# Kernel tuning notes

Hardware: AMD Instinct MI355X
Metric: run time of the kernel (lower is better)

## Reference

```python
import jax, jax.numpy as jnp
import numpy as np

V, E, H, C = 100000, 300, 512, 3
SP, SH, B = 64, 32, 128


def lstm_scan(x, Wih, Whh, b):
    # x: [T, B, E]; PyTorch gate order i, f, g, o
    T, Bb, _ = x.shape
    Hh = Whh.shape[1]
    h0 = jnp.zeros((Bb, Hh), x.dtype)

    def step(carry, xt):
        h, c = carry
        g = xt @ Wih.T + h @ Whh.T + b
        i, f, gg, o = jnp.split(g, 4, axis=-1)
        c = jax.nn.sigmoid(f) * c + jax.nn.sigmoid(i) * jnp.tanh(gg)
        h = jax.nn.sigmoid(o) * jnp.tanh(c)
        return (h, c), h

    _, hs = jax.lax.scan(step, (h0, h0), x)
    return hs  # [T, B, H]


def setup_inputs() -> dict:
    key = jax.random.key(0)
    ks = jax.random.split(key, 20)
    inv_sqrt_h = 1.0 / np.sqrt(H).astype(np.float32)

    def u(k, shape, scale):
        return (jax.random.uniform(k, shape, jnp.float32) * 2.0 - 1.0) * scale

    embed_table = jax.random.normal(ks[4], (V, E), jnp.float32) * 0.1
    embed_table = embed_table.at[0].set(0.0)  # padding_idx=0
    return {
        "premise": jax.random.randint(ks[0], (SP, B), 1, V),
        "premise_len": jax.random.randint(ks[1], (B,), 1, SP + 1),
        "hypothesis": jax.random.randint(ks[2], (SH, B), 1, V),
        "hypothesis_len": jax.random.randint(ks[3], (B,), 1, SH + 1),
        "embed_table": embed_table,
        "p_Wih": u(ks[5], (4 * H, E), inv_sqrt_h),
        "p_Whh": u(ks[6], (4 * H, H), inv_sqrt_h),
        "p_b": u(ks[7], (4 * H,), inv_sqrt_h),
        "h_Wih": u(ks[8], (4 * H, E), inv_sqrt_h),
        "h_Whh": u(ks[9], (4 * H, H), inv_sqrt_h),
        "h_b": u(ks[10], (4 * H,), inv_sqrt_h),
        "m_Wih": u(ks[11], (4 * H, 2 * H), inv_sqrt_h),
        "m_Whh": u(ks[12], (4 * H, H), inv_sqrt_h),
        "m_b": u(ks[13], (4 * H,), inv_sqrt_h),
        "w_e": jax.random.uniform(ks[14], (H,), jnp.float32),
        "Ws": u(ks[15], (H, H), np.sqrt(6.0 / (2 * H)).astype(np.float32)),
        "Wt": u(ks[16], (H, H), np.sqrt(6.0 / (2 * H)).astype(np.float32)),
        "Wm": u(ks[17], (H, H), np.sqrt(6.0 / (2 * H)).astype(np.float32)),
        "fc_W": u(ks[18], (C, H), np.sqrt(6.0 / (H + C)).astype(np.float32)),
        "fc_b": jnp.zeros((C,), jnp.float32),
    }


def reference(premise, premise_len, hypothesis, hypothesis_len, embed_table,
              p_Wih, p_Whh, p_b, h_Wih, h_Whh, h_b, m_Wih, m_Whh, m_b,
              w_e, Ws, Wt, Wm, fc_W, fc_b):
    Sp, Bb = premise.shape
    Sh = hypothesis.shape[0]
    Hh = Ws.shape[0]

    # Encoder LSTMs; emulate pack/pad: outputs past length are zeros
    h_s = lstm_scan(embed_table[premise], p_Wih, p_Whh, p_b)  # [Sp,B,H]
    h_s = h_s * (jnp.arange(Sp)[:, None] < premise_len[None, :]).astype(h_s.dtype)[:, :, None]
    h_t = lstm_scan(embed_table[hypothesis], h_Wih, h_Whh, h_b)  # [Sh,B,H]
    h_t = h_t * (jnp.arange(Sh)[:, None] < hypothesis_len[None, :]).astype(h_t.dtype)[:, :, None]

    Ws_hs = jnp.einsum('sbe,he->sbh', h_s, Ws)  # precompute premise projection

    def step(carry, inputs):
        h_m, c_m, h_last = carry
        h_t_k, k = inputs
        q = h_t_k @ Wt.T + h_m @ Wm.T                              # [B,H]
        e = jnp.einsum('sbh,h->sb', jnp.tanh(Ws_hs + q[None]), w_e)  # [Sp,B]
        alpha = jax.nn.softmax(e, axis=0)                           # softmax over premise (no mask, as in original)
        a_k = jnp.einsum('sb,sbh->bh', alpha, h_s)
        m_k = jnp.concatenate([a_k, h_t_k], axis=1)                 # [B,2H]
        g = m_k @ m_Wih.T + h_m @ m_Whh.T + m_b
        i, f, gg, o = jnp.split(g, 4, axis=-1)
        c_new = jax.nn.sigmoid(f) * c_m + jax.nn.sigmoid(i) * jnp.tanh(gg)
        h_new = jax.nn.sigmoid(o) * jnp.tanh(c_new)
        h_last = jnp.where((k + 1 == hypothesis_len)[:, None], h_new, h_last)
        return (h_new, c_new, h_last), None

    z = jnp.zeros((Bb, Hh), h_s.dtype)
    (_, _, h_last), _ = jax.lax.scan(step, (z, z, z), (h_t, jnp.arange(Sh)))
    return h_last @ fc_W.T + fc_b  # [B, C]
```

## Files before the change

### kernel.cpp

```cpp
#include <hip/hip_runtime.h>


#define NWG 256
#define TPB 512

typedef float f8v __attribute__((ext_vector_type(8)));

#define O_XPP      0ull
#define O_HTMW     0ull
#define O_HTWT     8388608ull
#define O_WSHS     10485760ull
#define O_XPH      16777216ull
#define O_HST      25165824ull
#define O_HS2      29360128ull
#define O_HTT      33554432ull
#define O_WIHTP    35651584ull
#define O_WIHTH    36265984ull
#define O_WHHPP    36880384ull
#define O_WHHPH    37928960ull
#define O_DW       38977536ull
#define O_WST      41074688ull
#define O_WTT      41336832ull
#define O_MWIHRT   41598976ull
#define O_BPP      42647552ull
#define O_BPH      42649600ull
#define O_BPM      42651648ull
#define O_HT2      42653696ull
#define O_HMT2     42784768ull
#define O_QBUF     42915840ull
#define O_AK2      42981376ull
#define O_HLAST    43046912ull
#define WS_FLOATS  43112448ull

__device__ unsigned g_FE[NWG * 16];
__device__ unsigned g_FA[NWG * 16];
__device__ unsigned g_FB[NWG * 16];
__device__ unsigned g_FD[NWG * 16];

struct Params {
  const int* premise; const int* plen; const int* hyp; const int* hlen;
  const float* embed;
  const float* pWih; const float* pWhh; const float* pb;
  const float* hWih; const float* hWhh; const float* hb;
  const float* mWih; const float* mWhh; const float* mb;
  const float* we; const float* Ws; const float* Wt; const float* Wm;
  const float* fcW; const float* fcb;
  float* out; float* ws;
};

__device__ __forceinline__ float2 sysld2(const float* p){
  unsigned long long u = __hip_atomic_load((const unsigned long long*)p,
      __ATOMIC_RELAXED, __HIP_MEMORY_SCOPE_SYSTEM);
  union { unsigned long long u; float2 f; } c; c.u = u; return c.f;
}
__device__ __forceinline__ void sysst(float* p, float v){
  union { float f; unsigned u; } c; c.f = v;
  __hip_atomic_store((unsigned*)p, c.u, __ATOMIC_RELAXED, __HIP_MEMORY_SCOPE_SYSTEM);
}
__device__ __forceinline__ void fbump(unsigned* a, unsigned v){
  __hip_atomic_store(a, v, __ATOMIC_RELAXED, __HIP_MEMORY_SCOPE_SYSTEM);
}
__device__ __forceinline__ unsigned fread_(const unsigned* a){
  return __hip_atomic_load(a, __ATOMIC_RELAXED, __HIP_MEMORY_SCOPE_SYSTEM);
}
__device__ __forceinline__ void waitflag(const unsigned* a, unsigned tgt){
  while ((int)(fread_(a) - tgt) < 0) __builtin_amdgcn_s_sleep(2);
}

__device__ __forceinline__ float sigf(float x){ return 1.0f/(1.0f + __expf(-x)); }
__device__ __forceinline__ float tanhf_(float x){ return 2.0f/(1.0f + __expf(-2.0f*x)) - 1.0f; }

__device__ __forceinline__ float wsum(float v){
  #pragma unroll
  for (int o = 32; o > 0; o >>= 1) v += __shfl_xor(v, o, 64);
  return v;
}
__device__ __forceinline__ float wmaxr(float v){
  #pragma unroll
  for (int o = 32; o > 0; o >>= 1) v = fmaxf(v, __shfl_xor(v, o, 64));
  return v;
}

__global__ __launch_bounds__(TPB) void k_s0(Params p){
  const int tid0 = blockIdx.x * TPB + threadIdx.x;
  const int stride = gridDim.x * TPB;
  float* const ws = p.ws;
  float* const WihTp  = ws + O_WIHTP;
  float* const WihTh  = ws + O_WIHTH;
  float* const WhhPP  = ws + O_WHHPP;
  float* const WhhPH  = ws + O_WHHPH;
  float* const DW     = ws + O_DW;
  float* const WsT    = ws + O_WST;
  float* const WtT    = ws + O_WTT;
  float* const mWihRT = ws + O_MWIHRT;
  float* const bpP    = ws + O_BPP;
  float* const bpH    = ws + O_BPH;
  float* const bpM    = ws + O_BPM;

  for (int idx = tid0; idx < 300*2048; idx += stride){
    int e = idx >> 11, jp = idx & 2047;
    int oc = (jp & 3) * 512 + (jp >> 2);
    WihTp[idx] = p.pWih[(size_t)oc*300 + e];
    WihTh[idx] = p.hWih[(size_t)oc*300 + e];
  }
  for (int idx = tid0; idx < 1024*512*2; idx += stride){
    int g = idx & 1, k = (idx >> 1) & 511, pp = idx >> 10;
    int hc = pp >> 1, gp = pp & 1, oc = (gp*2+g)*512 + hc;
    WhhPP[idx] = p.pWhh[(size_t)oc*512 + k];
    WhhPH[idx] = p.hWhh[(size_t)oc*512 + k];
  }
  for (int idx = tid0; idx < 1024*1024*2; idx += stride){
    int g = idx & 1, k = (idx >> 1) & 1023, pp = idx >> 11;
    int hc = pp >> 1, gp = pp & 1, oc = (gp*2+g)*512 + hc;
    DW[idx] = (k < 512) ? p.mWih[(size_t)oc*1024 + k]
                        : p.mWhh[(size_t)oc*512 + (k - 512)];
  }
  for (int idx = tid0; idx < 512*512; idx += stride){
    int k = idx >> 9, h = idx & 511;
    WsT[idx] = p.Ws[(size_t)h*512 + k];
    WtT[idx] = p.Wt[(size_t)h*512 + k];
  }
  for (int idx = tid0; idx < 512*2048; idx += stride){
    int k = idx >> 11, jp = idx & 2047;
    int oc = (jp & 3) * 512 + (jp >> 2);
    mWihRT[idx] = p.mWih[(size_t)oc*1024 + 512 + k];
  }
  for (int idx = tid0; idx < 2048; idx += stride){
    int oc = (idx & 3) * 512 + (idx >> 2);
    bpP[idx] = p.pb[oc]; bpH[idx] = p.hb[oc]; bpM[idx] = p.mb[oc];
  }
}

__global__ __launch_bounds__(TPB) void k_s1(Params p){
  const int tid = threadIdx.x, lane = tid & 63, wave = tid >> 6;
  const int gwave = blockIdx.x * 8 + wave;
  const int wstride = gridDim.x * 8;
  float* const ws = p.ws;
  float* const XPp   = ws + O_XPP;
  float* const XPh   = ws + O_XPH;
  const float* WihTp = ws + O_WIHTP;
  const float* WihTh = ws + O_WIHTH;
  const float* bpP   = ws + O_BPP;
  const float* bpH   = ws + O_BPH;

  for (int task = gwave; task < 6144; task += wstride){
    const bool prem = task < 4096;
    int rb, cb;
    if (prem){ cb = task >> 10; rb = task & 1023; }
    else { int t2 = task - 4096; cb = t2 >> 9; rb = t2 & 511; }
    const int r0 = rb * 8;
    const int* toks = prem ? p.premise : p.hyp;
    const float* wT = prem ? WihTp : WihTh;
    const float* bias = prem ? bpP : bpH;
    float* outp = prem ? XPp : XPh;
    const int j0 = cb * 512 + lane * 8;
    const float* xr[8];
    #pragma unroll
    for (int r = 0; r < 8; ++r) xr[r] = p.embed + (size_t)toks[r0 + r] * 300;
    f8v bias8 = *(const f8v*)(bias + j0);
    float acc[8][8];
    #pragma unroll
    for (int r = 0; r < 8; ++r){
      #pragma unroll
      for (int i = 0; i < 8; ++i) acc[r][i] = 0.f;
    }
    for (int e = 0; e < 300; ++e){
      f8v w8 = *(const f8v*)(wT + (size_t)e * 2048 + j0);
      #pragma unroll
      for (int r = 0; r < 8; ++r){
        float xv = xr[r][e];
        #pragma unroll
        for (int i = 0; i < 8; ++i) acc[r][i] += xv * w8[i];
      }
    }
    #pragma unroll
    for (int r = 0; r < 8; ++r){
      f8v o8;
      #pragma unroll
      for (int i = 0; i < 8; ++i) o8[i] = acc[r][i] + bias8[i];
      *(f8v*)(outp + (size_t)(r0 + r) * 2048 + j0) = o8;
    }
  }
}

__device__ void lstm_enc(int wg, int tid, int cg, int bg, int T,
    const float* __restrict__ XP, const float* __restrict__ WPair,
    const int* __restrict__ lens, float* hbuf,
    float* __restrict__ houtT, float* __restrict__ hout2, float* lds,
    unsigned B)
{
  const int b8 = tid & 7, hc32 = (tid >> 3) & 31, gp = tid >> 8;
  const int b = bg*8 + b8, hc = cg*32 + hc32;
  const float* wrow = WPair + (size_t)(hc*2 + gp) * 1024;
  const int mylen = lens[b];
  const int sb = tid >> 6, sk = (tid & 63) * 8;
  float* stage = lds;
  float* xch   = lds + 8*516;
  float c_reg = 0.f;

  for (int t = 0; t < T; ++t){
    const float* hin  = hbuf + (size_t)(t & 1) * 65536;
    float*       hout = hbuf + (size_t)((t + 1) & 1) * 65536;
    if (t > 0){
      if (tid < 16) waitflag(&g_FE[(unsigned)(bg*16 + tid)*16], B + t);
      __syncthreads();
      const float* src = hin + (size_t)(bg*8 + sb)*512 + sk;
      float2 v0 = sysld2(src), v1 = sysld2(src+2), v2 = sysld2(src+4), v3 = sysld2(src+6);
      float* dst = stage + sb*516 + sk;
      float4 w0 = {v0.x, v0.y, v1.x, v1.y};
      float4 w1 = {v2.x, v2.y, v3.x, v3.y};
      *(float4*)dst = w0; *(float4*)(dst+4) = w1;
    }
    __syncthreads();
    float a0 = 0.f, a1 = 0.f;
    if (t > 0){
      const float* hr = stage + b8*516;
      #pragma unroll 2
      for (int k = 0; k < 512; k += 4){
        float4 h4 = *(const float4*)(hr + k);
        float4 wA = *(const float4*)(wrow + k*2);
        float4 wB = *(const float4*)(wrow + k*2 + 4);
        a0 += h4.x*wA.x + h4.y*wA.z + h4.z*wB.x + h4.w*wB.z;
        a1 += h4.x*wA.y + h4.y*wA.w + h4.z*wB.y + h4.w*wB.w;
      }
    }
    float2 xg = *(const float2*)(XP + ((size_t)t*128 + b)*2048 + hc*4 + gp*2);
    a0 += xg.x; a1 += xg.y;
    if (gp == 1){ xch[(b8*32+hc32)*2+0] = a0; xch[(b8*32+hc32)*2+1] = a1; }
    __syncthreads();
    if (gp == 0){
      float gg = xch[(b8*32+hc32)*2+0], go = xch[(b8*32+hc32)*2+1];
      float iv = sigf(a0), fv = sigf(a1), gv = tanhf_(gg), ov = sigf(go);
      c_reg = fv * c_reg + iv * gv;
      float hv = ov * tanhf_(c_reg);
      sysst(hout + (size_t)b*512 + hc, hv);
      float hm = (t < mylen) ? hv : 0.f;
      houtT[((size_t)t*512 + hc)*128 + b] = hm;
      if (hout2) hout2[((size_t)t*128 + b)*512 + hc] = hm;
    }
    __syncthreads();
    if (tid == 0) fbump(&g_FE[wg*16], B + t + 1);
  }
}

__global__ __launch_bounds__(TPB, 2) void k_encp(Params p){
  const int wg = blockIdx.x, tid = threadIdx.x;
  const int cg = wg & 15, bg = wg >> 4;
  __shared__ float lds[4640];
  __shared__ unsigned shB;
  if (tid == 0) shB = fread_(&g_FE[wg*16]);
  __syncthreads();
  lstm_enc(wg, tid, cg, bg, 64, p.ws + O_XPP, p.ws + O_WHHPP, p.plen,
           p.ws + O_HT2, p.ws + O_HST, p.ws + O_HS2, lds, shB);
}
__global__ __launch_bounds__(TPB, 2) void k_ench(Params p){
  const int wg = blockIdx.x, tid = threadIdx.x;
  const int cg = wg & 15, bg = wg >> 4;
  __shared__ float lds[4640];
  __shared__ unsigned shB;
  if (tid == 0) shB = fread_(&g_FE[wg*16]);
  __syncthreads();
  lstm_enc(wg, tid, cg, bg, 32, p.ws + O_XPH, p.ws + O_WHHPH, p.hlen,
           p.ws + O_HT2, p.ws + O_HTT, nullptr, lds, shB);
}

__global__ __launch_bounds__(TPB) void k_s4(Params p){
  const int tid = threadIdx.x, lane = tid & 63, wave = tid >> 6;
  const int gwave = blockIdx.x * 8 + wave;
  const int wstride = gridDim.x * 8;
  float* const ws = p.ws;
  const float* h_sT   = ws + O_HST;
  const float* h_tT   = ws + O_HTT;
  const float* WsT    = ws + O_WST;
  const float* WtT    = ws + O_WTT;
  const float* mWihRT = ws + O_MWIHRT;
  const float* bpM    = ws + O_BPM;
  float* const Ws_hs  = ws + O_WSHS;
  float* const htWt   = ws + O_HTWT;
  float* const htmW   = ws + O_HTMW;

  for (int task = gwave; task < 3584; task += wstride){
    const float* src; const float* wT; const float* bias; float* outp;
    int rb, cb, cols;
    if (task < 1024){ rb = task;        cb = 0;            src = h_sT; wT = WsT;    bias = nullptr; outp = Ws_hs; cols = 512; }
    else if (task < 1536){ rb = task-1024; cb = 0;         src = h_tT; wT = WtT;    bias = nullptr; outp = htWt;  cols = 512; }
    else { int t2 = task - 1536; cb = t2 >> 9; rb = t2 & 511; src = h_tT; wT = mWihRT; bias = bpM;  outp = htmW;  cols = 2048; }
    const int r0 = rb * 8;
    const int j0 = cb * 512 + lane * 8;
    const float* xr[8];
    #pragma unroll
    for (int r = 0; r < 8; ++r){
      int row = r0 + r;
      xr[r] = src + (size_t)(row >> 7) * 65536 + (row & 127);
    }
    f8v bias8 = {0,0,0,0,0,0,0,0};
    if (bias) bias8 = *(const f8v*)(bias + j0);
    float acc[8][8];
    #pragma unroll
    for (int r = 0; r < 8; ++r){
      #pragma unroll
      for (int i = 0; i < 8; ++i) acc[r][i] = 0.f;
    }
    for (int k = 0; k < 512; ++k){
      f8v w8 = *(const f8v*)(wT + (size_t)k * cols + j0);
      #pragma unroll
      for (int r = 0; r < 8; ++r){
        float xv = xr[r][(size_t)k * 128];
        #pragma unroll
        for (int i = 0; i < 8; ++i) acc[r][i] += xv * w8[i];
      }
    }
    #pragma unroll
    for (int r = 0; r < 8; ++r){
      f8v o8;
      #pragma unroll
      for (int i = 0; i < 8; ++i) o8[i] = acc[r][i] + bias8[i];
      *(f8v*)(outp + (size_t)(r0 + r) * (size_t)cols + j0) = o8;
    }
  }
}

__global__ __launch_bounds__(TPB, 2) void k_match(Params p){
  const int wg = blockIdx.x, tid = threadIdx.x;
  const int lane = tid & 63, wave = tid >> 6;
  const int cg = wg & 15, bg = wg >> 4;
  __shared__ float lds[8736];
  __shared__ unsigned shB;
  if (tid == 0) shB = fread_(&g_FD[wg*16]);
  __syncthreads();
  const unsigned B = shB;

  float* const ws = p.ws;
  const float* htmW  = ws + O_HTMW;
  const float* htWt  = ws + O_HTWT;
  const float* Ws_hs = ws + O_WSHS;
  const float* h_s2  = ws + O_HS2;
  const float* DW    = ws + O_DW;
  float* const hmT2  = ws + O_HMT2;
  float* const qbuf  = ws + O_QBUF;
  float* const ak2   = ws + O_AK2;
  float* const hlast = ws + O_HLAST;

  const int b8 = tid & 7, hc32 = (tid >> 3) & 31, gp = tid >> 8;
  const int mb_ = bg*8 + b8, mhc = cg*32 + hc32;
  const float* dwrow = DW + (size_t)(mhc*2 + gp) * 2048;
  const int hyplen_b = p.hlen[mb_];
  const int sb = tid >> 6, sk = (tid & 63) * 8;
  float* stage  = lds;
  float* xchA   = lds + 8*516;
  float* stage2 = lds;
  float* xch2   = lds + 8*1028;
  float cm_reg = 0.f, hl_reg = 0.f;

  for (int k = 0; k < 32; ++k){
    const float* hmin  = hmT2 + (size_t)(k & 1) * 65536;
    float*       hmout = hmT2 + (size_t)((k + 1) & 1) * 65536;

    if (tid < 16) waitflag(&g_FD[(unsigned)(bg*16 + tid)*16], B + k);
    else if (tid < 24) waitflag(&g_FB[(unsigned)(bg*8 + tid - 16)*16], B + k);
    __syncthreads();
    if (k > 0){
      const float* src = hmin + (size_t)(bg*8 + sb)*512 + sk;
      float2 v0 = sysld2(src), v1 = sysld2(src+2), v2 = sysld2(src+4), v3 = sysld2(src+6);
      float* dst = stage + sb*516 + sk;
      float4 w0 = {v0.x, v0.y, v1.x, v1.y};
      float4 w1 = {v2.x, v2.y, v3.x, v3.y};
      *(float4*)dst = w0; *(float4*)(dst+4) = w1;
    }
    __syncthreads();
    {
      const int c32 = (tid >> 3) & 31, half = tid >> 8;
      const int c = cg*32 + c32;
      float a = 0.f;
      if (k > 0){
        const float* hr = stage + b8*516 + half*256;
        const float* wr = p.Wm + (size_t)c*512 + half*256;
        #pragma unroll 2
        for (int kk = 0; kk < 256; kk += 4){
          float4 h4 = *(const float4*)(hr + kk);
          float4 w4 = *(const float4*)(wr + kk);
          a += h4.x*w4.x + h4.y*w4.y + h4.z*w4.z + h4.w*w4.w;
        }
      }
      if (half == 1) xchA[c32*8 + b8] = a;
      __syncthreads();
      if (half == 0){
        float v = a + xchA[c32*8 + b8] + htWt[((size_t)k*128 + mb_)*512 + c];
        sysst(qbuf + (size_t)mb_*512 + c, v);
      }
    }
    __syncthreads();
    if (tid == 0) fbump(&g_FA[wg*16], B + k + 1);

    if (wg < 128){
      const int bb = wg;
      if (tid < 16) waitflag(&g_FA[(unsigned)((bb >> 3)*16 + tid)*16], B + k + 1);
      else if (tid < 32) waitflag(&g_FD[(unsigned)((bb >> 3)*16 + tid - 16)*16], B + k);
      __syncthreads();
      const float* qb = qbuf + (size_t)bb*512 + lane*8;
      float2 qa = sysld2(qb), qbv = sysld2(qb+2), qc = sysld2(qb+4), qd = sysld2(qb+6);
      float4 q0 = {qa.x, qa.y, qbv.x, qbv.y};
      float4 q1 = {qc.x, qc.y, qd.x, qd.y};
      float4 e0 = *(const float4*)(p.we + lane*8);
      float4 e1 = *(const float4*)(p.we + lane*8 + 4);
      #pragma unroll
      for (int si = 0; si < 8; ++si){
        int s = wave*8 + si;
        const float* wsr = Ws_hs + ((size_t)s*128 + bb)*512 + lane*8;
        float4 s0 = *(const float4*)wsr;
        float4 s1 = *(const float4*)(wsr + 4);
        float v = tanhf_(s0.x + q0.x)*e0.x + tanhf_(s0.y + q0.y)*e0.y
                + tanhf_(s0.z + q0.z)*e0.z + tanhf_(s0.w + q0.w)*e0.w
                + tanhf_(s1.x + q1.x)*e1.x + tanhf_(s1.y + q1.y)*e1.y
                + tanhf_(s1.z + q1.z)*e1.z + tanhf_(s1.w + q1.w)*e1.w;
        v = wsum(v);
        if (lane == 0) lds[s] = v;
      }
      __syncthreads();
      if (wave == 0){
        float v = lds[lane];
        float m = wmaxr(v);
        float ex = __expf(v - m);
        float sm = wsum(ex);
        lds[64 + lane] = ex / sm;
      }
      __syncthreads();
      {
        float acc = 0.f;
        const float* hsb = h_s2 + (size_t)bb*512 + tid;
        #pragma unroll 4
        for (int s = 0; s < 64; s += 4){
          float4 al = *(const float4*)(lds + 64 + s);
          acc += al.x * hsb[(size_t)(s+0)*65536]
               + al.y * hsb[(size_t)(s+1)*65536]
               + al.z * hsb[(size_t)(s+2)*65536]
               + al.w * hsb[(size_t)(s+3)*65536];
        }
        sysst(ak2 + (size_t)bb*512 + tid, acc);
      }
      __syncthreads();
      if (tid == 0) fbump(&g_FB[wg*16], B + k + 1);
    }

    if (tid < 8) waitflag(&g_FB[(unsigned)(bg*8 + tid)*16], B + k + 1);
    __syncthreads();
    {
      const int sb2 = tid >> 6, c0 = (tid & 63) * 16;
      float* dst = stage2 + sb2*1028 + c0;
      if (c0 < 512){
        const float* src = ak2 + (size_t)(bg*8 + sb2)*512 + c0;
        #pragma unroll
        for (int i = 0; i < 16; i += 4){
          float2 va = sysld2(src + i), vb = sysld2(src + i + 2);
          float4 w = {va.x, va.y, vb.x, vb.y};
          *(float4*)(dst + i) = w;
        }
      } else if (k > 0){
        const float* src = hmin + (size_t)(bg*8 + sb2)*512 + (c0 - 512);
        #pragma unroll
        for (int i = 0; i < 16; i += 4){
          float2 va = sysld2(src + i), vb = sysld2(src + i + 2);
          float4 w = {va.x, va.y, vb.x, vb.y};
          *(float4*)(dst + i) = w;
        }
      } else {
        float4 z = {0.f, 0.f, 0.f, 0.f};
        #pragma unroll
        for (int i = 0; i < 16; i += 4) *(float4*)(dst + i) = z;
      }
    }
    __syncthreads();
    {
      float a0 = 0.f, a1 = 0.f;
      const float* hr = stage2 + b8*1028;
      #pragma unroll 2
      for (int kk = 0; kk < 1024; kk += 4){
        float4 h4 = *(const float4*)(hr + kk);
        float4 wA = *(const float4*)(dwrow + kk*2);
        float4 wB = *(const float4*)(dwrow + kk*2 + 4);
        a0 += h4.x*wA.x + h4.y*wA.z + h4.z*wB.x + h4.w*wB.z;
        a1 += h4.x*wA.y + h4.y*wA.w + h4.z*wB.y + h4.w*wB.w;
      }
      float2 xg = *(const float2*)(htmW + ((size_t)k*128 + mb_)*2048 + mhc*4 + gp*2);
      a0 += xg.x; a1 += xg.y;
      if (gp == 1){ xch2[(b8*32+hc32)*2+0] = a0; xch2[(b8*32+hc32)*2+1] = a1; }
      __syncthreads();
      if (gp == 0){
        float gg = xch2[(b8*32+hc32)*2+0], go = xch2[(b8*32+hc32)*2+1];
        float iv = sigf(a0), fv = sigf(a1), gv = tanhf_(gg), ov = sigf(go);
        cm_reg = fv * cm_reg + iv * gv;
        float hv = ov * tanhf_(cm_reg);
        sysst(hmout + (size_t)mb_*512 + mhc, hv);
        if (k + 1 == hyplen_b) hl_reg = hv;
      }
    }
    __syncthreads();
    if (tid == 0) fbump(&g_FD[wg*16], B + k + 1);
  }

  if (gp == 0) sysst(hlast + (size_t)mb_*512 + mhc, hl_reg);
  __syncthreads();
  if (tid == 0){
    fbump(&g_FD[wg*16], B + 40);
    fbump(&g_FA[wg*16], B + 40);
    fbump(&g_FB[wg*16], B + 40);
  }

  if (wg == 0){
    if (tid < NWG) waitflag(&g_FD[(unsigned)tid*16], B + 40);
    __syncthreads();
    for (int o = wave; o < 384; o += 8){
      int bb = o / 3, cls = o - bb*3;
      const float* hr = hlast + (size_t)bb*512 + lane*8;
      const float* wr = p.fcW + (size_t)cls*512 + lane*8;
      float2 ha = sysld2(hr), hb = sysld2(hr+2), hc2 = sysld2(hr+4), hd = sysld2(hr+6);
      float4 w0 = *(const float4*)wr, w1 = *(const float4*)(wr + 4);
      float v = ha.x*w0.x + ha.y*w0.y + hb.x*w0.z + hb.y*w0.w
              + hc2.x*w1.x + hc2.y*w1.y + hd.x*w1.z + hd.y*w1.w;
      v = wsum(v);
      if (lane == 0) p.out[o] = v + p.fcb[cls];
    }
  }
}

extern "C" void kernel_launch(void* const* d_in, const int* in_sizes, int n_in,
                              void* d_out, int out_size, void* d_ws, size_t ws_size,
                              hipStream_t stream) {
  if (ws_size < WS_FLOATS * sizeof(float)) return;
  Params prm;
  prm.premise = (const int*)d_in[0];
  prm.plen    = (const int*)d_in[1];
  prm.hyp     = (const int*)d_in[2];
  prm.hlen    = (const int*)d_in[3];
  prm.embed   = (const float*)d_in[4];
  prm.pWih    = (const float*)d_in[5];
  prm.pWhh    = (const float*)d_in[6];
  prm.pb      = (const float*)d_in[7];
  prm.hWih    = (const float*)d_in[8];
  prm.hWhh    = (const float*)d_in[9];
  prm.hb      = (const float*)d_in[10];
  prm.mWih    = (const float*)d_in[11];
  prm.mWhh    = (const float*)d_in[12];
  prm.mb      = (const float*)d_in[13];
  prm.we      = (const float*)d_in[14];
  prm.Ws      = (const float*)d_in[15];
  prm.Wt      = (const float*)d_in[16];
  prm.Wm      = (const float*)d_in[17];
  prm.fcW     = (const float*)d_in[18];
  prm.fcb     = (const float*)d_in[19];
  prm.out     = (float*)d_out;
  prm.ws      = (float*)d_ws;

  k_s0   <<<dim3(1024), dim3(TPB), 0, stream>>>(prm);
  k_s1   <<<dim3(768),  dim3(TPB), 0, stream>>>(prm);
  k_encp <<<dim3(NWG),  dim3(TPB), 0, stream>>>(prm);
  k_ench <<<dim3(NWG),  dim3(TPB), 0, stream>>>(prm);
  k_s4   <<<dim3(448),  dim3(TPB), 0, stream>>>(prm);
  k_match<<<dim3(NWG),  dim3(TPB), 0, stream>>>(prm);
}
```

Before: 4.305 ms.

## Run premise and hypothesis encoders concurrently and fuse query step into attention workgroups

After: 10.17 ms. +136.2%, slower.

```diff
diff --git a/kernel.cpp b/kernel.cpp
--- a/kernel.cpp
+++ b/kernel.cpp
@@ -27,13 +27,12 @@
 #define O_BPM      42651648ull
 #define O_HT2      42653696ull
 #define O_HMT2     42784768ull
-#define O_QBUF     42915840ull
 #define O_AK2      42981376ull
 #define O_HLAST    43046912ull
-#define WS_FLOATS  43112448ull
+#define O_WMT      43112448ull
+#define WS_FLOATS  43374592ull
 
 __device__ unsigned g_FE[NWG * 16];
-__device__ unsigned g_FA[NWG * 16];
 __device__ unsigned g_FB[NWG * 16];
 __device__ unsigned g_FD[NWG * 16];
 
@@ -92,6 +91,7 @@
   float* const DW     = ws + O_DW;
   float* const WsT    = ws + O_WST;
   float* const WtT    = ws + O_WTT;
+  float* const WmT    = ws + O_WMT;
   float* const mWihRT = ws + O_MWIHRT;
   float* const bpP    = ws + O_BPP;
   float* const bpH    = ws + O_BPH;
@@ -103,9 +103,9 @@
     WihTp[idx] = p.pWih[(size_t)oc*300 + e];
     WihTh[idx] = p.hWih[(size_t)oc*300 + e];
   }
-  for (int idx = tid0; idx < 1024*512*2; idx += stride){
-    int g = idx & 1, k = (idx >> 1) & 511, pp = idx >> 10;
-    int hc = pp >> 1, gp = pp & 1, oc = (gp*2+g)*512 + hc;
+  for (int idx = tid0; idx < 512*4*512; idx += stride){
+    int k = idx & 511, g = (idx >> 9) & 3, hc = idx >> 11;
+    int oc = g*512 + hc;
     WhhPP[idx] = p.pWhh[(size_t)oc*512 + k];
     WhhPH[idx] = p.hWhh[(size_t)oc*512 + k];
   }
@@ -119,6 +119,7 @@
     int k = idx >> 9, h = idx & 511;
     WsT[idx] = p.Ws[(size_t)h*512 + k];
     WtT[idx] = p.Wt[(size_t)h*512 + k];
+    WmT[idx] = p.Wm[(size_t)h*512 + k];
   }
   for (int idx = tid0; idx < 512*2048; idx += stride){
     int k = idx >> 11, jp = idx & 2047;
@@ -183,85 +184,74 @@
   }
 }
 
-__device__ void lstm_enc(int wg, int tid, int cg, int bg, int T,
-    const float* __restrict__ XP, const float* __restrict__ WPair,
-    const int* __restrict__ lens, float* hbuf,
-    float* __restrict__ houtT, float* __restrict__ hout2, float* lds,
-    unsigned B)
-{
-  const int b8 = tid & 7, hc32 = (tid >> 3) & 31, gp = tid >> 8;
-  const int b = bg*8 + b8, hc = cg*32 + hc32;
-  const float* wrow = WPair + (size_t)(hc*2 + gp) * 1024;
+__global__ __launch_bounds__(TPB, 2) void k_enc(Params p){
+  const int wg = blockIdx.x, tid = threadIdx.x;
+  const bool prem = wg < 128;
+  const int lw = prem ? wg : wg - 128;
+  const int cg = lw & 15, bg = lw >> 4;
+  const int T = prem ? 64 : 32;
+  const float* XP  = p.ws + (prem ? O_XPP : O_XPH);
+  const float* Wg  = p.ws + (prem ? O_WHHPP : O_WHHPH);
+  const int* lens  = prem ? p.plen : p.hlen;
+  float* hbuf      = p.ws + (prem ? O_HT2 : O_HMT2);
+  float* houtT     = p.ws + (prem ? O_HST : O_HTT);
+  float* hout2     = prem ? (p.ws + O_HS2) : nullptr;
+  __shared__ float stage[16*520];
+  __shared__ unsigned shB;
+  if (tid == 0) shB = fread_(&g_FE[wg*16]);
+  __syncthreads();
+  const unsigned B = shB;
+  const int b16 = tid >> 5, hc32 = tid & 31;
+  const int b = bg*16 + b16, hc = cg*32 + hc32;
+  const float* wrow = Wg + (size_t)hc * 2048;
   const int mylen = lens[b];
-  const int sb = tid >> 6, sk = (tid & 63) * 8;
-  float* stage = lds;
-  float* xch   = lds + 8*516;
+  const int srow = tid & 15, schunk = (tid >> 4) & 31;
+  const int flagbase = (prem ? 0 : 128) + bg*16;
   float c_reg = 0.f;
 
   for (int t = 0; t < T; ++t){
-    const float* hin  = hbuf + (size_t)(t & 1) * 65536;
+    const float* hin = hbuf + (size_t)(t & 1) * 65536;
     float*       hout = hbuf + (size_t)((t + 1) & 1) * 65536;
     if (t > 0){
-      if (tid < 16) waitflag(&g_FE[(unsigned)(bg*16 + tid)*16], B + t);
-      __syncthreads();
-      const float* src = hin + (size_t)(bg*8 + sb)*512 + sk;
-      float2 v0 = sysld2(src), v1 = sysld2(src+2), v2 = sysld2(src+4), v3 = sysld2(src+6);
-      float* dst = stage + sb*516 + sk;
-      float4 w0 = {v0.x, v0.y, v1.x, v1.y};
-      float4 w1 = {v2.x, v2.y, v3.x, v3.y};
-      *(float4*)dst = w0; *(float4*)(dst+4) = w1;
+      if (tid < 16) waitflag(&g_FE[(unsigned)(flagbase + tid)*16], B + t);
+      __syncthreads();
+      const float* src = hin + (size_t)(bg*16 + srow)*512 + schunk*16;
+      float* dst = stage + srow*520 + schunk*16;
+      #pragma unroll
+      for (int i = 0; i < 16; i += 4){
+        float2 va = sysld2(src + i), vb = sysld2(src + i + 2);
+        float4 w = {va.x, va.y, vb.x, vb.y};
+        *(float4*)(dst + i) = w;
+      }
     }
     __syncthreads();
-    float a0 = 0.f, a1 = 0.f;
+    float4 xg = *(const float4*)(XP + ((size_t)t*128 + b)*2048 + hc*4);
+    float a0 = xg.x, a1 = xg.y, a2 = xg.z, a3 = xg.w;
     if (t > 0){
-      const float* hr = stage + b8*516;
+      const float* hr = stage + b16*520;
       #pragma unroll 2
       for (int k = 0; k < 512; k += 4){
         float4 h4 = *(const float4*)(hr + k);
-        float4 wA = *(const float4*)(wrow + k*2);
-        float4 wB = *(const float4*)(wrow + k*2 + 4);
-        a0 += h4.x*wA.x + h4.y*wA.z + h4.z*wB.x + h4.w*wB.z;
-        a1 += h4.x*wA.y + h4.y*wA.w + h4.z*wB.y + h4.w*wB.w;
-      }
-    }
-    float2 xg = *(const float2*)(XP + ((size_t)t*128 + b)*2048 + hc*4 + gp*2);
-    a0 += xg.x; a1 += xg.y;
-    if (gp == 1){ xch[(b8*32+hc32)*2+0] = a0; xch[(b8*32+hc32)*2+1] = a1; }
-    __syncthreads();
-    if (gp == 0){
-      float gg = xch[(b8*32+hc32)*2+0], go = xch[(b8*32+hc32)*2+1];
-      float iv = sigf(a0), fv = sigf(a1), gv = tanhf_(gg), ov = sigf(go);
-      c_reg = fv * c_reg + iv * gv;
-      float hv = ov * tanhf_(c_reg);
-      sysst(hout + (size_t)b*512 + hc, hv);
-      float hm = (t < mylen) ? hv : 0.f;
-      houtT[((size_t)t*512 + hc)*128 + b] = hm;
-      if (hout2) hout2[((size_t)t*128 + b)*512 + hc] = hm;
-    }
+        float4 w0 = *(const float4*)(wrow + k);
+        float4 w1 = *(const float4*)(wrow + 512 + k);
+        float4 w2 = *(const float4*)(wrow + 1024 + k);
+        float4 w3 = *(const float4*)(wrow + 1536 + k);
+        a0 += h4.x*w0.x + h4.y*w0.y + h4.z*w0.z + h4.w*w0.w;
+        a1 += h4.x*w1.x + h4.y*w1.y + h4.z*w1.z + h4.w*w1.w;
+        a2 += h4.x*w2.x + h4.y*w2.y + h4.z*w2.z + h4.w*w2.w;
+        a3 += h4.x*w3.x + h4.y*w3.y + h4.z*w3.z + h4.w*w3.w;
+      }
+    }
+    float iv = sigf(a0), fv = sigf(a1), gv = tanhf_(a2), ov = sigf(a3);
+    c_reg = fv * c_reg + iv * gv;
+    float hv = ov * tanhf_(c_reg);
+    sysst(hout + (size_t)b*512 + hc, hv);
+    float hm = (t < mylen) ? hv : 0.f;
+    houtT[((size_t)t*512 + hc)*128 + b] = hm;
+    if (hout2) hout2[((size_t)t*128 + b)*512 + hc] = hm;
     __syncthreads();
     if (tid == 0) fbump(&g_FE[wg*16], B + t + 1);
   }
-}
-
-__global__ __launch_bounds__(TPB, 2) void k_encp(Params p){
-  const int wg = blockIdx.x, tid = threadIdx.x;
-  const int cg = wg & 15, bg = wg >> 4;
-  __shared__ float lds[4640];
-  __shared__ unsigned shB;
-  if (tid == 0) shB = fread_(&g_FE[wg*16]);
-  __syncthreads();
-  lstm_enc(wg, tid, cg, bg, 64, p.ws + O_XPP, p.ws + O_WHHPP, p.plen,
-           p.ws + O_HT2, p.ws + O_HST, p.ws + O_HS2, lds, shB);
-}
-__global__ __launch_bounds__(TPB, 2) void k_ench(Params p){
-  const int wg = blockIdx.x, tid = threadIdx.x;
-  const int cg = wg & 15, bg = wg >> 4;
-  __shared__ float lds[4640];
-  __shared__ unsigned shB;
-  if (tid == 0) shB = fread_(&g_FE[wg*16]);
-  __syncthreads();
-  lstm_enc(wg, tid, cg, bg, 32, p.ws + O_XPH, p.ws + O_WHHPH, p.hlen,
-           p.ws + O_HT2, p.ws + O_HTT, nullptr, lds, shB);
 }
 
 __global__ __launch_bounds__(TPB) void k_s4(Params p){
@@ -324,6 +314,8 @@
   const int wg = blockIdx.x, tid = threadIdx.x;
   const int lane = tid & 63, wave = tid >> 6;
   const int cg = wg & 15, bg = wg >> 4;
+  const bool bcrole = cg < 8;
+  const int bb = bg*8 + cg;
   __shared__ float lds[8736];
   __shared__ unsigned shB;
   if (tid == 0) shB = fread_(&g_FD[wg*16]);
@@ -336,18 +328,15 @@
   const float* Ws_hs = ws + O_WSHS;
   const float* h_s2  = ws + O_HS2;
   const float* DW    = ws + O_DW;
+  const float* WmT   = ws + O_WMT;
   float* const hmT2  = ws + O_HMT2;
-  float* const qbuf  = ws + O_QBUF;
   float* const ak2   = ws + O_AK2;
   float* const hlast = ws + O_HLAST;
 
-  const int b8 = tid & 7, hc32 = (tid >> 3) & 31, gp = tid >> 8;
-  const int mb_ = bg*8 + b8, mhc = cg*32 + hc32;
+  const int b8 = tid & 7, hc32d = (tid >> 3) & 31, gp = tid >> 8;
+  const int mb_ = bg*8 + b8, mhc = cg*32 + hc32d;
   const float* dwrow = DW + (size_t)(mhc*2 + gp) * 2048;
   const int hyplen_b = p.hlen[mb_];
-  const int sb = tid >> 6, sk = (tid & 63) * 8;
-  float* stage  = lds;
-  float* xchA   = lds + 8*516;
   float* stage2 = lds;
   float* xch2   = lds + 8*1028;
   float cm_reg = 0.f, hl_reg = 0.f;
@@ -356,51 +345,33 @@
     const float* hmin  = hmT2 + (size_t)(k & 1) * 65536;
     float*       hmout = hmT2 + (size_t)((k + 1) & 1) * 65536;
 
-    if (tid < 16) waitflag(&g_FD[(unsigned)(bg*16 + tid)*16], B + k);
-    else if (tid < 24) waitflag(&g_FB[(unsigned)(bg*8 + tid - 16)*16], B + k);
-    __syncthreads();
-    if (k > 0){
-      const float* src = hmin + (size_t)(bg*8 + sb)*512 + sk;
-      float2 v0 = sysld2(src), v1 = sysld2(src+2), v2 = sysld2(src+4), v3 = sysld2(src+6);
-      float* dst = stage + sb*516 + sk;
-      float4 w0 = {v0.x, v0.y, v1.x, v1.y};
-      float4 w1 = {v2.x, v2.y, v3.x, v3.y};
-      *(float4*)dst = w0; *(float4*)(dst+4) = w1;
-    }
-    __syncthreads();
-    {
-      const int c32 = (tid >> 3) & 31, half = tid >> 8;
-      const int c = cg*32 + c32;
-      float a = 0.f;
+    if (bcrole){
       if (k > 0){
-        const float* hr = stage + b8*516 + half*256;
-        const float* wr = p.Wm + (size_t)c*512 + half*256;
-        #pragma unroll 2
-        for (int kk = 0; kk < 256; kk += 4){
-          float4 h4 = *(const float4*)(hr + kk);
-          float4 w4 = *(const float4*)(wr + kk);
-          a += h4.x*w4.x + h4.y*w4.y + h4.z*w4.z + h4.w*w4.w;
+        if (tid < 16) waitflag(&g_FD[(unsigned)(bg*16 + tid)*16], B + k);
+        __syncthreads();
+        if (tid < 256){
+          float2 v = sysld2(hmin + (size_t)bb*512 + tid*2);
+          lds[tid*2] = v.x; lds[tid*2+1] = v.y;
         }
       }
-      if (half == 1) xchA[c32*8 + b8] = a;
-      __syncthreads();
-      if (half == 0){
-        float v = a + xchA[c32*8 + b8] + htWt[((size_t)k*128 + mb_)*512 + c];
-        sysst(qbuf + (size_t)mb_*512 + c, v);
-      }
-    }
-    __syncthreads();
-    if (tid == 0) fbump(&g_FA[wg*16], B + k + 1);
-
-    if (wg < 128){
-      const int bb = wg;
-      if (tid < 16) waitflag(&g_FA[(unsigned)((bb >> 3)*16 + tid)*16], B + k + 1);
-      else if (tid < 32) waitflag(&g_FD[(unsigned)((bb >> 3)*16 + tid - 16)*16], B + k);
-      __syncthreads();
-      const float* qb = qbuf + (size_t)bb*512 + lane*8;
-      float2 qa = sysld2(qb), qbv = sysld2(qb+2), qc = sysld2(qb+4), qd = sysld2(qb+6);
-      float4 q0 = {qa.x, qa.y, qbv.x, qbv.y};
-      float4 q1 = {qc.x, qc.y, qd.x, qd.y};
+      __syncthreads();
+      float qv = htWt[((size_t)k*128 + bb)*512 + tid];
+      if (k > 0){
+        float q0 = 0.f, q1 = 0.f, q2 = 0.f, q3 = 0.f;
+        for (int kk = 0; kk < 512; kk += 4){
+          q0 += lds[kk]   * WmT[(size_t)(kk)  *512 + tid];
+          q1 += lds[kk+1] * WmT[(size_t)(kk+1)*512 + tid];
+          q2 += lds[kk+2] * WmT[(size_t)(kk+2)*512 + tid];
+          q3 += lds[kk+3] * WmT[(size_t)(kk+3)*512 + tid];
+        }
+        qv += (q0 + q1) + (q2 + q3);
+      }
+      __syncthreads();
+      lds[512 + tid] = qv;
+      __syncthreads();
+      float q8[8];
+      #pragma unroll
+      for (int j = 0; j < 8; ++j) q8[j] = lds[512 + lane*8 + j];
       float4 e0 = *(const float4*)(p.we + lane*8);
       float4 e1 = *(const float4*)(p.we + lane*8 + 4);
       #pragma unroll
@@ -409,20 +380,20 @@
         const float* wsr = Ws_hs + ((size_t)s*128 + bb)*512 + lane*8;
         float4 s0 = *(const float4*)wsr;
         float4 s1 = *(const float4*)(wsr + 4);
-        float v = tanhf_(s0.x + q0.x)*e0.x + tanhf_(s0.y + q0.y)*e0.y
-                + tanhf_(s0.z + q0.z)*e0.z + tanhf_(s0.w + q0.w)*e0.w
-                + tanhf_(s1.x + q1.x)*e1.x + tanhf_(s1.y + q1.y)*e1.y
-                + tanhf_(s1.z + q1.z)*e1.z + tanhf_(s1.w + q1.w)*e1.w;
+        float v = tanhf_(s0.x + q8[0])*e0.x + tanhf_(s0.y + q8[1])*e0.y
+                + tanhf_(s0.z + q8[2])*e0.z + tanhf_(s0.w + q8[3])*e0.w
+                + tanhf_(s1.x + q8[4])*e1.x + tanhf_(s1.y + q8[5])*e1.y
+                + tanhf_(s1.z + q8[6])*e1.z + tanhf_(s1.w + q8[7])*e1.w;
         v = wsum(v);
-        if (lane == 0) lds[s] = v;
+        if (lane == 0) lds[1024 + s] = v;
       }
       __syncthreads();
       if (wave == 0){
-        float v = lds[lane];
+        float v = lds[1024 + lane];
         float m = wmaxr(v);
         float ex = __expf(v - m);
         float sm = wsum(ex);
-        lds[64 + lane] = ex / sm;
+        lds[1088 + lane] = ex / sm;
       }
       __syncthreads();
       {
@@ -430,7 +401,7 @@
         const float* hsb = h_s2 + (size_t)bb*512 + tid;
         #pragma unroll 4
         for (int s = 0; s < 64; s += 4){
-          float4 al = *(const float4*)(lds + 64 + s);
+          float4 al = *(const float4*)(lds + 1088 + s);
           acc += al.x * hsb[(size_t)(s+0)*65536]
                + al.y * hsb[(size_t)(s+1)*65536]
                + al.z * hsb[(size_t)(s+2)*65536]
@@ -442,7 +413,11 @@
       if (tid == 0) fbump(&g_FB[wg*16], B + k + 1);
     }
 
-    if (tid < 8) waitflag(&g_FB[(unsigned)(bg*8 + tid)*16], B + k + 1);
+    if (!bcrole && k > 0){
+      if (tid < 16) waitflag(&g_FD[(unsigned)(bg*16 + tid)*16], B + k);
+    }
+    if (tid >= 16 && tid < 24)
+      waitflag(&g_FB[(unsigned)(bg*16 + (tid - 16))*16], B + k + 1);
     __syncthreads();
     {
       const int sb2 = tid >> 6, c0 = (tid & 63) * 16;
@@ -483,10 +458,10 @@
       }
       float2 xg = *(const float2*)(htmW + ((size_t)k*128 + mb_)*2048 + mhc*4 + gp*2);
       a0 += xg.x; a1 += xg.y;
-      if (gp == 1){ xch2[(b8*32+hc32)*2+0] = a0; xch2[(b8*32+hc32)*2+1] = a1; }
+      if (gp == 1){ xch2[(b8*32+hc32d)*2+0] = a0; xch2[(b8*32+hc32d)*2+1] = a1; }
       __syncthreads();
       if (gp == 0){
-        float gg = xch2[(b8*32+hc32)*2+0], go = xch2[(b8*32+hc32)*2+1];
+        float gg = xch2[(b8*32+hc32d)*2+0], go = xch2[(b8*32+hc32d)*2+1];
         float iv = sigf(a0), fv = sigf(a1), gv = tanhf_(gg), ov = sigf(go);
         cm_reg = fv * cm_reg + iv * gv;
         float hv = ov * tanhf_(cm_reg);
@@ -502,7 +477,6 @@
   __syncthreads();
   if (tid == 0){
     fbump(&g_FD[wg*16], B + 40);
-    fbump(&g_FA[wg*16], B + 40);
     fbump(&g_FB[wg*16], B + 40);
   }
 
@@ -510,8 +484,8 @@
     if (tid < NWG) waitflag(&g_FD[(unsigned)tid*16], B + 40);
     __syncthreads();
     for (int o = wave; o < 384; o += 8){
-      int bb = o / 3, cls = o - bb*3;
-      const float* hr = hlast + (size_t)bb*512 + lane*8;
+      int bbq = o / 3, cls = o - bbq*3;
+      const float* hr = hlast + (size_t)bbq*512 + lane*8;
       const float* wr = p.fcW + (size_t)cls*512 + lane*8;
       float2 ha = sysld2(hr), hb = sysld2(hr+2), hc2 = sysld2(hr+4), hd = sysld2(hr+6);
       float4 w0 = *(const float4*)wr, w1 = *(const float4*)(wr + 4);
@@ -553,8 +527,7 @@
 
   k_s0   <<<dim3(1024), dim3(TPB), 0, stream>>>(prm);
   k_s1   <<<dim3(768),  dim3(TPB), 0, stream>>>(prm);
-  k_encp <<<dim3(NWG),  dim3(TPB), 0, stream>>>(prm);
-  k_ench <<<dim3(NWG),  dim3(TPB), 0, stream>>>(prm);
+  k_enc  <<<dim3(NWG),  dim3(TPB), 0, stream>>>(prm);
   k_s4   <<<dim3(448),  dim3(TPB), 0, stream>>>(prm);
   k_match<<<dim3(NWG),  dim3(TPB), 0, stream>>>(prm);
 }
```
